# Performance work log

Measured on AMD Instinct MI355X. Metric: run time of the kernel, lower is better.

Reference implementation:

```python
import jax, jax.numpy as jnp
import numpy as np

E = 8        # num_experts
K = 2        # top_k routing
D = 1024     # d_model
F = 4096     # expert hidden (ffn) dim
EPS = 1e-5


def _layernorm(h, g, b):
    # h: [E, T, C]; g, b: [E, C]
    mu = h.mean(axis=-1, keepdims=True)
    var = ((h - mu) ** 2).mean(axis=-1, keepdims=True)
    return (h - mu) * jax.lax.rsqrt(var + EPS) * g[:, None, :] + b[:, None, :]


def setup_inputs() -> dict:
    key = jax.random.key(0)
    ks = jax.random.split(key, 8)
    B, S = 2, 2048
    x = jax.random.normal(ks[0], (B, S, D), dtype=jnp.float32)
    Wr = jax.random.normal(ks[1], (D, E), dtype=jnp.float32) / np.sqrt(D)
    br = jnp.zeros((E,), dtype=jnp.float32)
    W1 = jax.random.normal(ks[2], (E, D, F), dtype=jnp.float32) / np.sqrt(D)
    b1 = jnp.zeros((E, F), dtype=jnp.float32)
    g1 = jnp.ones((E, F), dtype=jnp.float32)
    be1 = jnp.zeros((E, F), dtype=jnp.float32)
    W2 = jax.random.normal(ks[3], (E, F, D), dtype=jnp.float32) / np.sqrt(F)
    b2 = jnp.zeros((E, D), dtype=jnp.float32)
    g2 = jnp.ones((E, D), dtype=jnp.float32)
    be2 = jnp.zeros((E, D), dtype=jnp.float32)
    return {"x": x, "Wr": Wr, "br": br, "W1": W1, "b1": b1, "g1": g1,
            "be1": be1, "W2": W2, "b2": b2, "g2": g2, "be2": be2}


def reference(x, Wr, br, W1, b1, g1, be1, W2, b2, g2, be2):
    B, S, _ = x.shape
    xt = x.reshape(-1, D)                       # [T, D] token matrix
    # --- router + sampler: top-k softmax probs, renormalized over the k slots
    logits = xt @ Wr + br                       # [T, E]
    p = jax.nn.softmax(logits, axis=-1)
    probs, idx = jax.lax.top_k(p, K)            # [T, K]
    probs = probs / probs.sum(axis=-1, keepdims=True)
    # --- experts layer 1: Linear -> relu -> LayerNorm, per expert
    h = jnp.einsum('td,edf->etf', xt, W1) + b1[:, None, :]   # [E, T, F]
    h = _layernorm(jax.nn.relu(h), g1, be1)
    # --- experts layer 2: Linear -> relu -> LayerNorm
    y = jnp.einsum('etf,efd->etd', h, W2) + b2[:, None, :]   # [E, T, D]
    y = _layernorm(jax.nn.relu(y), g2, be2)
    # --- weighted scatter-combine: gate[t,e] = sum_k 1[idx[t,k]==e] * probs[t,k]
    gate = (jax.nn.one_hot(idx, E, dtype=x.dtype) * probs[..., None]).sum(axis=1)  # [T, E]
    out = jnp.einsum('te,etd->td', gate, y)     # index_add combine, dense form
    return out.reshape(B, S, D)
```

## Files before the change

kernel.cpp:

```cpp
#include <hip/hip_runtime.h>


#define E_N 8
#define TOPK 2
#define DM 1024
#define FF 4096
#define NTOK 4096
#define NA 8192
#define LN_EPS 1e-5f
#define NBX 128

typedef __attribute__((ext_vector_type(4))) float f32x4;
typedef __attribute__((ext_vector_type(8))) short short8;

__device__ __forceinline__ unsigned short f2bf(float f) {
    unsigned int u = __builtin_bit_cast(unsigned int, f);
    u = (u + 0x7FFFu + ((u >> 16) & 1u)) >> 16;
    return (unsigned short)u;
}
__device__ __forceinline__ float bf2f(unsigned short h) {
    unsigned int u = ((unsigned int)h) << 16;
    return __builtin_bit_cast(float, u);
}
__device__ __forceinline__ void unp(unsigned int u, float& lo, float& hi) {
    lo = bf2f((unsigned short)(u & 0xffffu));
    hi = bf2f((unsigned short)(u >> 16));
}
__device__ __forceinline__ unsigned int pk(float lo, float hi) {
    return (unsigned int)f2bf(lo) | ((unsigned int)f2bf(hi) << 16);
}

__device__ __forceinline__ void gload16(const unsigned short* g, unsigned short* lds) {
    __builtin_amdgcn_global_load_lds(
        (const __attribute__((address_space(1))) unsigned int*)g,
        (__attribute__((address_space(3))) unsigned int*)lds, 16, 0, 0);
}

__device__ __forceinline__ void transpose128x64(const float* __restrict__ s, int sld,
                                                unsigned short* __restrict__ d, int dld,
                                                float* tile) {
    int tid = threadIdx.x;
    int rr = tid >> 4, cc = (tid & 15) * 4;
    float4 v[8];
#pragma unroll
    for (int p = 0; p < 8; p++)
        v[p] = *(const float4*)(s + (size_t)(rr + p * 16) * sld + cc);
#pragma unroll
    for (int p = 0; p < 8; p++) {
        int r = rr + p * 16;
        *(float4*)&tile[r * 64 + (cc ^ ((r >> 5) << 3))] = v[p];
    }
    __syncthreads();
    int o = tid >> 2;
    int k0 = (tid & 3) * 32;
    int q8 = (tid & 3) << 3;
    const float* base = tile + (size_t)k0 * 64 + (o ^ q8);
    float f[32];
#pragma unroll
    for (int m = 0; m < 32; m++) f[m] = base[m * 64];
    unsigned int ov[16];
#pragma unroll
    for (int m = 0; m < 16; m++) ov[m] = pk(f[2 * m], f[2 * m + 1]);
    unsigned short* dp = d + (size_t)o * dld + k0;
    *(uint4*)(dp)      = *(uint4*)&ov[0];
    *(uint4*)(dp + 8)  = *(uint4*)&ov[4];
    *(uint4*)(dp + 16) = *(uint4*)&ov[8];
    *(uint4*)(dp + 24) = *(uint4*)&ov[12];
}


__global__ __launch_bounds__(256) void k_prep(
        const float* __restrict__ W1, const float* __restrict__ W2,
        unsigned short* __restrict__ W1T, unsigned short* __restrict__ W2T,
        const float* __restrict__ x, const float* __restrict__ Wr,
        const float* __restrict__ br, unsigned short* __restrict__ xb,
        int* __restrict__ topk_idx, float* __restrict__ topk_p)
{
    __shared__ float tile[128 * 64];
    int z = blockIdx.z;
    int tid = threadIdx.x;

    if (z == 16) {
        int wv = tid >> 6, lane = tid & 63;
        int t = blockIdx.x * 4 + wv;
        const float* xr = x + (size_t)t * DM;
        unsigned short* xbr = xb + (size_t)t * DM;
        float4 xv[4];
#pragma unroll
        for (int p = 0; p < 4; p++)
            xv[p] = *(const float4*)(xr + p * 256 + lane * 4);
#pragma unroll
        for (int p = 0; p < 4; p++) {
            uint2 pkd; pkd.x = pk(xv[p].x, xv[p].y); pkd.y = pk(xv[p].z, xv[p].w);
            *(uint2*)(xbr + p * 256 + lane * 4) = pkd;
        }
        float a0=0,a1=0,a2=0,a3=0,a4=0,a5=0,a6=0,a7=0;
#pragma unroll
        for (int p = 0; p < 4; p++) {
            int d0 = p * 256 + lane * 4;
            float xs[4] = {xv[p].x, xv[p].y, xv[p].z, xv[p].w};
#pragma unroll
            for (int j = 0; j < 4; j++) {
                const float4* wp = (const float4*)(Wr + (d0 + j) * 8);
                float4 w0 = wp[0], w1 = wp[1];
                a0 += xs[j] * w0.x; a1 += xs[j] * w0.y; a2 += xs[j] * w0.z; a3 += xs[j] * w0.w;
                a4 += xs[j] * w1.x; a5 += xs[j] * w1.y; a6 += xs[j] * w1.z; a7 += xs[j] * w1.w;
            }
        }
#pragma unroll
        for (int off = 32; off; off >>= 1) {
            a0 += __shfl_xor(a0, off); a1 += __shfl_xor(a1, off);
            a2 += __shfl_xor(a2, off); a3 += __shfl_xor(a3, off);
            a4 += __shfl_xor(a4, off); a5 += __shfl_xor(a5, off);
            a6 += __shfl_xor(a6, off); a7 += __shfl_xor(a7, off);
        }
        if (lane == 0) {
            float l[8] = {a0 + br[0], a1 + br[1], a2 + br[2], a3 + br[3],
                          a4 + br[4], a5 + br[5], a6 + br[6], a7 + br[7]};
            int i0 = 0;
#pragma unroll
            for (int e = 1; e < 8; e++) if (l[e] > l[i0]) i0 = e;
            int i1 = (i0 == 0) ? 1 : 0;
#pragma unroll
            for (int e = 0; e < 8; e++) if (e != i0 && l[e] > l[i1]) i1 = e;
            float p1 = expf(l[i1] - l[i0]);
            float s = 1.0f + p1;
            topk_idx[2 * t]     = i0;
            topk_idx[2 * t + 1] = i1;
            topk_p[2 * t]       = 1.0f / s;
            topk_p[2 * t + 1]   = p1 / s;
        }
        return;
    }

    if (blockIdx.x >= 512) return;

    if (z < 8) {
        int bx = blockIdx.x & 63, by = blockIdx.x >> 6;
        transpose128x64(
            W1 + (size_t)z * DM * FF + (size_t)(by * 128) * FF + bx * 64, FF,
            W1T + (size_t)z * DM * FF + (size_t)(bx * 64) * DM + by * 128, DM,
            tile);
    } else {
        int e = z - 8;
        int bx = blockIdx.x & 15, by = blockIdx.x >> 4;
        transpose128x64(
            W2 + (size_t)e * FF * DM + (size_t)(by * 128) * DM + bx * 64, DM,
            W2T + (size_t)e * DM * FF + (size_t)(bx * 64) * FF + by * 128, FF,
            tile);
    }
}


__global__ __launch_bounds__(256) void k_route2(const int* __restrict__ topk_idx,
        int* __restrict__ cnt, int* __restrict__ offs,
        int* __restrict__ assign_tok, int* __restrict__ assign_e,
        int* __restrict__ slot)
{
    __shared__ int h[8], base[8];
    int tid = threadIdx.x;
    if (tid < 8) h[tid] = 0;
    __syncthreads();
    int el[32];
#pragma unroll
    for (int i = 0; i < 32; i++) {
        int idx = tid * 32 + i;
        el[i] = topk_idx[idx];
        atomicAdd(&h[el[i]], 1);
    }
    __syncthreads();
    if (tid == 0) {
        int s = 0;
        for (int e = 0; e < E_N; e++) { offs[e] = s; cnt[e] = h[e]; base[e] = s; s += h[e]; }
        offs[E_N] = s;
    }
    __syncthreads();
    if (tid < 8) h[tid] = base[tid];
    __syncthreads();
#pragma unroll
    for (int i = 0; i < 32; i++) {
        int idx = tid * 32 + i;
        int e = el[i];
        int pos = atomicAdd(&h[e], 1);
        assign_tok[pos] = idx >> 1;
        assign_e[pos] = e;
        slot[idx] = pos;
    }
}


template<bool GATHER, bool EPI>
__global__ __launch_bounds__(256, 4) void k_gemm(
    const unsigned short* __restrict__ A,
    const unsigned short* __restrict__ BT,
    const float* __restrict__ bias,
    unsigned short* __restrict__ C,
    const int* __restrict__ cnt, const int* __restrict__ offs,
    const int* __restrict__ gather_tok,
    int Kslice, int N, int ldA, int ldB, int GX, int KS, size_t slicePitch)
{
    __shared__ __align__(1024) char lds[32768];

    int bid = blockIdx.x;
    int e = bid & 7;
    int lb = bid >> 3;
    int M = cnt[e];
    if (M <= 0) return;
    int off_e = offs[e];
    int nrows = (M + 127) >> 7;
    int ntiles = nrows * GX * KS;

    int tid = threadIdx.x;
    int wv = tid >> 6, lane = tid & 63;
    int lr = lane & 15, hi = lane >> 4;
    int mW = (wv >> 1) * 64, nW = (wv & 1) * 64;
    int colsw = ((lane & 7) ^ (lane >> 3)) * 8;
    int l3 = lane >> 3;
    int nt = Kslice >> 6;

    for (int t = lb; t < ntiles; t += NBX) {
        int r = t % nrows;
        int q = t / nrows;
        int xn = q % GX;
        int ks = q / GX;
        int m0 = r * 128;
        int n0 = xn * 128;
        int kbase = ks * Kslice;

        const unsigned short* aptr[4];
        const unsigned short* bptr[4];
#pragma unroll
        for (int i = 0; i < 4; i++) {
            int j = wv * 4 + i;
            int rr = m0 + j * 8 + l3; rr = (rr < M) ? rr : (M - 1);
            size_t arow = GATHER ? (size_t)gather_tok[off_e + rr] : (size_t)(off_e + rr);
            aptr[i] = A + arow * (size_t)ldA + kbase + colsw;
            int rb = n0 + j * 8 + l3;
            bptr[i] = BT + ((size_t)e * N + rb) * (size_t)ldB + kbase + colsw;
        }

        f32x4 acc[4][4];
        f32x4 zz = {0.f, 0.f, 0.f, 0.f};
#pragma unroll
        for (int mi = 0; mi < 4; mi++)
#pragma unroll
            for (int ni = 0; ni < 4; ni++) acc[mi][ni] = zz;

        for (int kt = 0; kt < nt; ++kt) {
            __syncthreads();
#pragma unroll
            for (int i = 0; i < 4; i++) {
                gload16(aptr[i] + kt * 64, (unsigned short*)(lds + (wv * 4 + i) * 1024));
                gload16(bptr[i] + kt * 64, (unsigned short*)(lds + 16384 + (wv * 4 + i) * 1024));
            }
            __syncthreads();
#pragma unroll
            for (int kss = 0; kss < 2; kss++) {
                int cb = (kss * 64 + hi * 16) ^ ((lr & 7) << 4);
                short8 afr[4], bfr[4];
#pragma unroll
                for (int ni = 0; ni < 4; ni++)
                    bfr[ni] = *(const short8*)(lds + 16384 + (nW + ni * 16 + lr) * 128 + cb);
#pragma unroll
                for (int mi = 0; mi < 4; mi++)
                    afr[mi] = *(const short8*)(lds + (mW + mi * 16 + lr) * 128 + cb);
                __builtin_amdgcn_s_setprio(1);
#pragma unroll
                for (int mi = 0; mi < 4; mi++)
#pragma unroll
                    for (int ni = 0; ni < 4; ni++)
                        acc[mi][ni] = __builtin_amdgcn_mfma_f32_16x16x32_bf16(
                            afr[mi], bfr[ni], acc[mi][ni], 0, 0, 0);
                __builtin_amdgcn_s_setprio(0);
            }
        }

        unsigned short* Cs = C + ks * slicePitch;
        float bv[4] = {0.f, 0.f, 0.f, 0.f};
        if (EPI) {
#pragma unroll
            for (int ni = 0; ni < 4; ni++)
                bv[ni] = bias[(size_t)e * N + (n0 + nW + ni * 16 + lr)];
        }
#pragma unroll
        for (int mi = 0; mi < 4; mi++) {
            int mb = m0 + mW + mi * 16 + hi * 4;
#pragma unroll
            for (int rr = 0; rr < 4; rr++) {
                int m = mb + rr;
                if (m < M) {
                    unsigned short* crow = Cs + (size_t)(off_e + m) * N;
#pragma unroll
                    for (int ni = 0; ni < 4; ni++) {
                        float v = acc[mi][ni][rr];
                        if (EPI) v = fmaxf(v + bv[ni], 0.0f);
                        crow[n0 + nW + ni * 16 + lr] = f2bf(v);
                    }
                }
            }
        }
    }
}


__global__ __launch_bounds__(256) void k_ln1(unsigned short* __restrict__ H,
        const float* __restrict__ g, const float* __restrict__ b,
        const int* __restrict__ assign_e)
{
    size_t a = blockIdx.x;
    int e = assign_e[a];
    unsigned short* row = H + a * FF;
    int tid = threadIdx.x;
    uint4 u0 = *(const uint4*)(row + tid * 16);
    uint4 u1 = *(const uint4*)(row + tid * 16 + 8);
    float v[16];
    unp(u0.x, v[0], v[1]);  unp(u0.y, v[2], v[3]);
    unp(u0.z, v[4], v[5]);  unp(u0.w, v[6], v[7]);
    unp(u1.x, v[8], v[9]);  unp(u1.y, v[10], v[11]);
    unp(u1.z, v[12], v[13]); unp(u1.w, v[14], v[15]);
    float s = 0.f, q = 0.f;
#pragma unroll
    for (int i = 0; i < 16; i++) { s += v[i]; q += v[i] * v[i]; }
#pragma unroll
    for (int off = 32; off; off >>= 1) { s += __shfl_xor(s, off); q += __shfl_xor(q, off); }
    __shared__ float red[8];
    int wv = tid >> 6, lane = tid & 63;
    if (lane == 0) { red[wv * 2] = s; red[wv * 2 + 1] = q; }
    __syncthreads();
    s = red[0] + red[2] + red[4] + red[6];
    q = red[1] + red[3] + red[5] + red[7];
    float mu = s * (1.0f / FF);
    float var = q * (1.0f / FF) - mu * mu;
    float rstd = rsqrtf(var + LN_EPS);
    const float* gg = g + (size_t)e * FF + tid * 16;
    const float* bb = b + (size_t)e * FF + tid * 16;
    float4 G0 = *(const float4*)(gg);      float4 G1 = *(const float4*)(gg + 4);
    float4 G2 = *(const float4*)(gg + 8);  float4 G3 = *(const float4*)(gg + 12);
    float4 B0 = *(const float4*)(bb);      float4 B1 = *(const float4*)(bb + 4);
    float4 B2 = *(const float4*)(bb + 8);  float4 B3 = *(const float4*)(bb + 12);
    float gvv[16] = {G0.x,G0.y,G0.z,G0.w,G1.x,G1.y,G1.z,G1.w,G2.x,G2.y,G2.z,G2.w,G3.x,G3.y,G3.z,G3.w};
    float bvv[16] = {B0.x,B0.y,B0.z,B0.w,B1.x,B1.y,B1.z,B1.w,B2.x,B2.y,B2.z,B2.w,B3.x,B3.y,B3.z,B3.w};
#pragma unroll
    for (int i = 0; i < 16; i++) v[i] = (v[i] - mu) * rstd * gvv[i] + bvv[i];
    u0.x = pk(v[0], v[1]);  u0.y = pk(v[2], v[3]);
    u0.z = pk(v[4], v[5]);  u0.w = pk(v[6], v[7]);
    u1.x = pk(v[8], v[9]);  u1.y = pk(v[10], v[11]);
    u1.z = pk(v[12], v[13]); u1.w = pk(v[14], v[15]);
    *(uint4*)(row + tid * 16) = u0;
    *(uint4*)(row + tid * 16 + 8) = u1;
}


__global__ __launch_bounds__(256) void k_comb(const unsigned short* __restrict__ Yp,
        const float* __restrict__ g, const float* __restrict__ b2,
        const float* __restrict__ be,
        const int* __restrict__ slot, const float* __restrict__ topk_p,
        const int* __restrict__ assign_e, float* __restrict__ out)
{
    int t = blockIdx.x;
    int s0 = slot[2 * t], s1 = slot[2 * t + 1];
    float p0 = topk_p[2 * t], p1 = topk_p[2 * t + 1];
    int e0 = assign_e[s0], e1 = assign_e[s1];
    int tid = threadIdx.x;
    int d = tid * 4;
    const unsigned short* Y1 = Yp + (size_t)NA * DM;
    uint2 ua0 = *(const uint2*)(Yp + (size_t)s0 * DM + d);
    uint2 ua1 = *(const uint2*)(Y1 + (size_t)s0 * DM + d);
    uint2 ub0 = *(const uint2*)(Yp + (size_t)s1 * DM + d);
    uint2 ub1 = *(const uint2*)(Y1 + (size_t)s1 * DM + d);
    float4 bza = *(const float4*)(b2 + (size_t)e0 * DM + d);
    float4 bzb = *(const float4*)(b2 + (size_t)e1 * DM + d);
    float x0, x1, y0, y1;
    float va[4], vb[4];
    unp(ua0.x, x0, x1); unp(ua1.x, y0, y1);
    va[0] = fmaxf(x0 + y0 + bza.x, 0.f); va[1] = fmaxf(x1 + y1 + bza.y, 0.f);
    unp(ua0.y, x0, x1); unp(ua1.y, y0, y1);
    va[2] = fmaxf(x0 + y0 + bza.z, 0.f); va[3] = fmaxf(x1 + y1 + bza.w, 0.f);
    unp(ub0.x, x0, x1); unp(ub1.x, y0, y1);
    vb[0] = fmaxf(x0 + y0 + bzb.x, 0.f); vb[1] = fmaxf(x1 + y1 + bzb.y, 0.f);
    unp(ub0.y, x0, x1); unp(ub1.y, y0, y1);
    vb[2] = fmaxf(x0 + y0 + bzb.z, 0.f); vb[3] = fmaxf(x1 + y1 + bzb.w, 0.f);

    float sa = 0.f, qa = 0.f, sb = 0.f, qb = 0.f;
#pragma unroll
    for (int i = 0; i < 4; i++) {
        sa += va[i]; qa += va[i] * va[i];
        sb += vb[i]; qb += vb[i] * vb[i];
    }
#pragma unroll
    for (int off = 32; off; off >>= 1) {
        sa += __shfl_xor(sa, off); qa += __shfl_xor(qa, off);
        sb += __shfl_xor(sb, off); qb += __shfl_xor(qb, off);
    }
    __shared__ float red[16];
    int wv = tid >> 6, lane = tid & 63;
    if (lane == 0) { red[wv*4+0]=sa; red[wv*4+1]=qa; red[wv*4+2]=sb; red[wv*4+3]=qb; }
    __syncthreads();
    sa = red[0] + red[4] + red[8]  + red[12];
    qa = red[1] + red[5] + red[9]  + red[13];
    sb = red[2] + red[6] + red[10] + red[14];
    qb = red[3] + red[7] + red[11] + red[15];
    float mua = sa * (1.0f / DM), vara = qa * (1.0f / DM) - mua * mua;
    float ra = rsqrtf(vara + LN_EPS);
    float mub = sb * (1.0f / DM), varb = qb * (1.0f / DM) - mub * mub;
    float rb = rsqrtf(varb + LN_EPS);
    float4 ga  = *(const float4*)(g + (size_t)e0 * DM + d);
    float4 ba  = *(const float4*)(be + (size_t)e0 * DM + d);
    float4 gb4 = *(const float4*)(g + (size_t)e1 * DM + d);
    float4 bb4 = *(const float4*)(be + (size_t)e1 * DM + d);
    float4 o;
    o.x = p0 * ((va[0] - mua) * ra * ga.x + ba.x) + p1 * ((vb[0] - mub) * rb * gb4.x + bb4.x);
    o.y = p0 * ((va[1] - mua) * ra * ga.y + ba.y) + p1 * ((vb[1] - mub) * rb * gb4.y + bb4.y);
    o.z = p0 * ((va[2] - mua) * ra * ga.z + ba.z) + p1 * ((vb[2] - mub) * rb * gb4.z + bb4.z);
    o.w = p0 * ((va[3] - mua) * ra * ga.w + ba.w) + p1 * ((vb[3] - mub) * rb * gb4.w + bb4.w);
    *(float4*)(out + (size_t)t * DM + d) = o;
}


extern "C" void kernel_launch(void* const* d_in, const int* in_sizes, int n_in,
                              void* d_out, int out_size, void* d_ws, size_t ws_size,
                              hipStream_t stream) {
    const float* x   = (const float*)d_in[0];
    const float* Wr  = (const float*)d_in[1];
    const float* br  = (const float*)d_in[2];
    const float* W1  = (const float*)d_in[3];
    const float* b1  = (const float*)d_in[4];
    const float* g1  = (const float*)d_in[5];
    const float* be1 = (const float*)d_in[6];
    const float* W2  = (const float*)d_in[7];
    const float* b2  = (const float*)d_in[8];
    const float* g2  = (const float*)d_in[9];
    const float* be2 = (const float*)d_in[10];
    float* out = (float*)d_out;

    char* w = (char*)d_ws;
    int*   cnt        = (int*)(w);
    int*   offs       = (int*)(w + 128);
    int*   topk_idx   = (int*)(w + 512);
    float* topk_p     = (float*)(w + 512 + (32 << 10));
    int*   assign_tok = (int*)(w + 512 + (64 << 10));
    int*   assign_e   = (int*)(w + 512 + (96 << 10));
    int*   slot       = (int*)(w + 512 + (128 << 10));
    unsigned short* xb  = (unsigned short*)(w + ((size_t)1 << 20));
    unsigned short* W1T = (unsigned short*)(w + ((size_t)9 << 20));
    unsigned short* W2T = (unsigned short*)(w + ((size_t)73 << 20));
    unsigned short* Hb  = (unsigned short*)(w + ((size_t)137 << 20));
    unsigned short* Yp  = (unsigned short*)(w + ((size_t)201 << 20));

    k_prep<<<dim3(1024, 1, 17), 256, 0, stream>>>(
        W1, W2, W1T, W2T, x, Wr, br, xb, topk_idx, topk_p);
    k_route2<<<1, 256, 0, stream>>>(topk_idx, cnt, offs, assign_tok, assign_e, slot);
    k_gemm<true, true><<<8 * NBX, 256, 0, stream>>>(
        xb, W1T, b1, Hb, cnt, offs, assign_tok, DM, FF, DM, DM, 32, 1, 0);
    k_ln1<<<NA, 256, 0, stream>>>(Hb, g1, be1, assign_e);
    k_gemm<false, false><<<8 * NBX, 256, 0, stream>>>(
        Hb, W2T, nullptr, Yp, cnt, offs, nullptr, FF / 2, DM, FF, FF, 8, 2,
        (size_t)NA * DM);
    k_comb<<<NTOK, 256, 0, stream>>>(Yp, g2, b2, be2, slot, topk_p, assign_e, out);
}
```

Measured before the change: 344.4 us.

## Pre-tile transposed expert weights into contiguous swizzled 128x64 bf16 blocks

```diff
diff --git a/kernel.cpp b/kernel.cpp
--- a/kernel.cpp
+++ b/kernel.cpp
@@ -36,36 +36,33 @@
         (__attribute__((address_space(3))) unsigned int*)lds, 16, 0, 0);
 }
 
-__device__ __forceinline__ void transpose128x64(const float* __restrict__ s, int sld,
-                                                unsigned short* __restrict__ d, int dld,
-                                                float* tile) {
-    int tid = threadIdx.x;
-    int rr = tid >> 4, cc = (tid & 15) * 4;
+__device__ __forceinline__ void make_btile(const float* __restrict__ s, int sld,
+                                           unsigned short* __restrict__ out,
+                                           float* tile) {
+    int tid = threadIdx.x;
+    int krow = tid >> 5, c4 = (tid & 31) * 4;
     float4 v[8];
 #pragma unroll
     for (int p = 0; p < 8; p++)
-        v[p] = *(const float4*)(s + (size_t)(rr + p * 16) * sld + cc);
-#pragma unroll
-    for (int p = 0; p < 8; p++) {
-        int r = rr + p * 16;
-        *(float4*)&tile[r * 64 + (cc ^ ((r >> 5) << 3))] = v[p];
-    }
-    __syncthreads();
-    int o = tid >> 2;
-    int k0 = (tid & 3) * 32;
-    int q8 = (tid & 3) << 3;
-    const float* base = tile + (size_t)k0 * 64 + (o ^ q8);
-    float f[32];
-#pragma unroll
-    for (int m = 0; m < 32; m++) f[m] = base[m * 64];
+        v[p] = *(const float4*)(s + (size_t)(krow + p * 8) * sld + c4);
+#pragma unroll
+    for (int p = 0; p < 8; p++)
+        *(float4*)&tile[(krow + p * 8) * 128 + c4] = v[p];
+    __syncthreads();
+    int r = tid >> 1, gh = (tid & 1) * 4;
+    const float* col = tile + r;
     unsigned int ov[16];
 #pragma unroll
-    for (int m = 0; m < 16; m++) ov[m] = pk(f[2 * m], f[2 * m + 1]);
-    unsigned short* dp = d + (size_t)o * dld + k0;
-    *(uint4*)(dp)      = *(uint4*)&ov[0];
-    *(uint4*)(dp + 8)  = *(uint4*)&ov[4];
-    *(uint4*)(dp + 16) = *(uint4*)&ov[8];
-    *(uint4*)(dp + 24) = *(uint4*)&ov[12];
+    for (int i = 0; i < 4; i++) {
+        int kb = ((gh + i) ^ (r & 7)) << 3;
+#pragma unroll
+        for (int ee = 0; ee < 8; ee += 2)
+            ov[i * 4 + (ee >> 1)] = pk(col[(kb + ee) * 128], col[(kb + ee + 1) * 128]);
+    }
+    unsigned short* dp = out + (size_t)r * 64 + gh * 8;
+#pragma unroll
+    for (int i = 0; i < 4; i++)
+        *(uint4*)(dp + i * 8) = *(uint4*)&ov[i * 4];
 }
 
 
@@ -76,7 +73,7 @@
         const float* __restrict__ br, unsigned short* __restrict__ xb,
         int* __restrict__ topk_idx, float* __restrict__ topk_p)
 {
-    __shared__ float tile[128 * 64];
+    __shared__ float tile[64 * 128];
     int z = blockIdx.z;
     int tid = threadIdx.x;
 
@@ -136,18 +133,14 @@
     if (blockIdx.x >= 512) return;
 
     if (z < 8) {
-        int bx = blockIdx.x & 63, by = blockIdx.x >> 6;
-        transpose128x64(
-            W1 + (size_t)z * DM * FF + (size_t)(by * 128) * FF + bx * 64, FF,
-            W1T + (size_t)z * DM * FF + (size_t)(bx * 64) * DM + by * 128, DM,
-            tile);
+        int nt = blockIdx.x >> 4, kt = blockIdx.x & 15;
+        make_btile(W1 + (size_t)z * DM * FF + (size_t)(kt * 64) * FF + nt * 128, FF,
+                   W1T + (((size_t)z * 32 + nt) * 16 + kt) * 8192, tile);
     } else {
         int e = z - 8;
-        int bx = blockIdx.x & 15, by = blockIdx.x >> 4;
-        transpose128x64(
-            W2 + (size_t)e * FF * DM + (size_t)(by * 128) * DM + bx * 64, DM,
-            W2T + (size_t)e * DM * FF + (size_t)(bx * 64) * FF + by * 128, FF,
-            tile);
+        int nt = blockIdx.x >> 6, kt = blockIdx.x & 63;
+        make_btile(W2 + (size_t)e * FF * DM + (size_t)(kt * 64) * DM + nt * 128, DM,
+                   W2T + (((size_t)e * 8 + nt) * 64 + kt) * 8192, tile);
     }
 }
 
@@ -197,7 +190,7 @@
     unsigned short* __restrict__ C,
     const int* __restrict__ cnt, const int* __restrict__ offs,
     const int* __restrict__ gather_tok,
-    int Kslice, int N, int ldA, int ldB, int GX, int KS, size_t slicePitch)
+    int Kslice, int N, int ldA, int NT, int KT, int GX, int KS, size_t slicePitch)
 {
     __shared__ __align__(1024) char lds[32768];
 
@@ -229,14 +222,14 @@
 
         const unsigned short* aptr[4];
         const unsigned short* bptr[4];
+        size_t btile = ((size_t)(e * NT + xn) * KT + (size_t)ks * nt) * 8192;
 #pragma unroll
         for (int i = 0; i < 4; i++) {
             int j = wv * 4 + i;
             int rr = m0 + j * 8 + l3; rr = (rr < M) ? rr : (M - 1);
             size_t arow = GATHER ? (size_t)gather_tok[off_e + rr] : (size_t)(off_e + rr);
             aptr[i] = A + arow * (size_t)ldA + kbase + colsw;
-            int rb = n0 + j * 8 + l3;
-            bptr[i] = BT + ((size_t)e * N + rb) * (size_t)ldB + kbase + colsw;
+            bptr[i] = BT + btile + j * 512 + lane * 8;
         }
 
         f32x4 acc[4][4];
@@ -251,7 +244,8 @@
 #pragma unroll
             for (int i = 0; i < 4; i++) {
                 gload16(aptr[i] + kt * 64, (unsigned short*)(lds + (wv * 4 + i) * 1024));
-                gload16(bptr[i] + kt * 64, (unsigned short*)(lds + 16384 + (wv * 4 + i) * 1024));
+                gload16(bptr[i] + (size_t)kt * 8192,
+                        (unsigned short*)(lds + 16384 + (wv * 4 + i) * 1024));
             }
             __syncthreads();
 #pragma unroll
@@ -451,10 +445,10 @@
         W1, W2, W1T, W2T, x, Wr, br, xb, topk_idx, topk_p);
     k_route2<<<1, 256, 0, stream>>>(topk_idx, cnt, offs, assign_tok, assign_e, slot);
     k_gemm<true, true><<<8 * NBX, 256, 0, stream>>>(
-        xb, W1T, b1, Hb, cnt, offs, assign_tok, DM, FF, DM, DM, 32, 1, 0);
+        xb, W1T, b1, Hb, cnt, offs, assign_tok, DM, FF, DM, 32, 16, 32, 1, 0);
     k_ln1<<<NA, 256, 0, stream>>>(Hb, g1, be1, assign_e);
     k_gemm<false, false><<<8 * NBX, 256, 0, stream>>>(
-        Hb, W2T, nullptr, Yp, cnt, offs, nullptr, FF / 2, DM, FF, FF, 8, 2,
+        Hb, W2T, nullptr, Yp, cnt, offs, nullptr, FF / 2, DM, FF, 8, 64, 8, 2,
         (size_t)NA * DM);
     k_comb<<<NTOK, 256, 0, stream>>>(Yp, g2, b2, be2, slot, topk_p, assign_e, out);
 }
```

New measurement: 332.0 us. 1.04x faster.
